# Optimization experiments

Measured on AMD Instinct MI355X. Metric: run time of the kernel, lower is better.

Reference implementation:

```python
import jax, jax.numpy as jnp
import numpy as np

QUANT = 6                      # quant bits
LEVELS = 2 ** QUANT - 1        # quant_levels = 63


def setup_inputs() -> dict:
    key = jax.random.key(0)
    k1, k2, k3 = jax.random.split(key, 3)
    B, C_in, C_out, H, W = 8, 256, 256, 64, 64
    x = jax.random.normal(k1, (B, C_in, H, W), dtype=jnp.float32)
    # 1x1 conv weight stored as [out_channels, in_channels] (kernel dims are 1)
    weight = jax.random.normal(k2, (C_out, C_in), dtype=jnp.float32) * 0.05
    bias = jax.random.normal(k3, (C_out,), dtype=jnp.float32) * 0.05
    return {"x": x, "weight": weight, "bias": bias}


def reference(x, weight, bias):
    """NoiseConv.forward with hard_weight set, mode='batch':
    channel_wise_quantize -> hardware_inference -> float cast.
    (Original computes in float64 on CUDA; here float32 for jit/accel friendliness.)
    """
    # --- channel_wise_quantize (input is detached in torch) ---
    xd = jax.lax.stop_gradient(x)
    cmax = jnp.max(xd, axis=1, keepdims=True)           # [B,1,H,W]
    cmin = jnp.min(xd, axis=1, keepdims=True)           # [B,1,H,W]
    scaling = (cmax - cmin) / LEVELS                    # [B,1,H,W]
    x_int = jnp.round((xd - cmin) / scaling).astype(jnp.int32)  # [B,C,H,W] in [0,63]
    bit_idx = jnp.arange(QUANT, dtype=jnp.int32)
    bits = ((x_int[..., None] >> bit_idx) & 1).astype(x.dtype)   # [B,C,H,W,Q] bitplanes

    # --- hardware_inference (batch mode): one 1x1 conv per bitplane, then
    # weighted recombination with 2^b. Fused here into a single einsum; the
    # math is identical since conv is linear and bitplane values are exact. ---
    base = (2.0 ** jnp.arange(QUANT)).astype(x.dtype)   # quant_base
    out_sum = jnp.einsum('bchwq,q,oc->bohw', bits, base, weight)  # [B,O,H,W]
    out_w = out_sum * scaling                           # per-pixel rescale

    # min-offset term: conv2d(cmin * ones_like(x_plane), weight, bias).
    # cmin is constant across input channels, so it equals cmin * sum_c(w) + bias.
    wsum = jnp.sum(weight, axis=1)                      # [O]
    out_w = out_w + cmin * wsum[None, :, None, None] + bias[None, :, None, None]

    return out_w.astype(jnp.float32)
```

## Files before the change

kernel.cpp:

```cpp
#include <hip/hip_runtime.h>
#include <stdint.h>

#define CI 256
#define CO 256
#define HW 4096
#define PT 64
#define QPAD 72

typedef __attribute__((ext_vector_type(8))) short short8;
typedef __attribute__((ext_vector_type(4))) float float4v;

__global__ void prep_kernel(const float* __restrict__ w,
                            ushort* __restrict__ w16,
                            float* __restrict__ wsum) {
    const int o = blockIdx.x;
    const int lane = threadIdx.x;
    float4 v = ((const float4*)(w + o * CI))[lane];
    auto cvt = [](float f) -> ushort {
        uint32_t u = __float_as_uint(f);
        return (ushort)((u + 0x7FFFu + ((u >> 16) & 1u)) >> 16);
    };
    ushort4 q;
    q.x = cvt(v.x); q.y = cvt(v.y); q.z = cvt(v.z); q.w = cvt(v.w);
    ((ushort4*)(w16 + o * CI))[lane] = q;
    float s = v.x + v.y + v.z + v.w;
    for (int off = 32; off >= 1; off >>= 1) s += __shfl_down(s, off);
    if (lane == 0) wsum[o] = s;
}

__global__ __launch_bounds__(256, 2)
void noise_conv_kernel(const float* __restrict__ x,
                       const ushort* __restrict__ w16,
                       const float* __restrict__ wsum,
                       const float* __restrict__ bias,
                       float* __restrict__ out) {
    __shared__ ushort Qlds[PT][QPAD];
    __shared__ float4 rmin4[16][16];
    __shared__ float4 rmax4[16][16];
    __shared__ float cmin_s[PT], s_s[PT], inv_s[PT];

    const int t = threadIdx.x;
    const int blk = blockIdx.x;
    const int img = blk >> 6;
    const int p0 = (blk & 63) * PT;
    const float* xb = x + (size_t)img * CI * HW + p0;
    float* outb = out + (size_t)img * CO * HW + p0;

    {
        const int pg = t & 15;
        const int slice = t >> 4;
        float4 vmin = make_float4(__builtin_inff(), __builtin_inff(),
                                  __builtin_inff(), __builtin_inff());
        float4 vmax = make_float4(-__builtin_inff(), -__builtin_inff(),
                                  -__builtin_inff(), -__builtin_inff());
        #pragma unroll
        for (int i = 0; i < 16; ++i) {
            const float4 v = ((const float4*)(xb + (size_t)(slice * 16 + i) * HW))[pg];
            vmin.x = fminf(vmin.x, v.x); vmax.x = fmaxf(vmax.x, v.x);
            vmin.y = fminf(vmin.y, v.y); vmax.y = fmaxf(vmax.y, v.y);
            vmin.z = fminf(vmin.z, v.z); vmax.z = fmaxf(vmax.z, v.z);
            vmin.w = fminf(vmin.w, v.w); vmax.w = fmaxf(vmax.w, v.w);
        }
        rmin4[slice][pg] = vmin;
        rmax4[slice][pg] = vmax;
    }
    __syncthreads();
    if (t < 16) {
        float4 mn = rmin4[0][t], mx = rmax4[0][t];
        for (int sl = 1; sl < 16; ++sl) {
            float4 a = rmin4[sl][t], b = rmax4[sl][t];
            mn.x = fminf(mn.x, a.x); mx.x = fmaxf(mx.x, b.x);
            mn.y = fminf(mn.y, a.y); mx.y = fmaxf(mx.y, b.y);
            mn.z = fminf(mn.z, a.z); mx.z = fmaxf(mx.z, b.z);
            mn.w = fminf(mn.w, a.w); mx.w = fmaxf(mx.w, b.w);
        }
        const float mnv[4] = {mn.x, mn.y, mn.z, mn.w};
        const float mxv[4] = {mx.x, mx.y, mx.z, mx.w};
        #pragma unroll
        for (int c = 0; c < 4; ++c) {
            const int p = t * 4 + c;
            const float cmin = mnv[c];
            const float sc = (mxv[c] - cmin) / 63.0f;
            cmin_s[p] = cmin;
            s_s[p] = sc;
            inv_s[p] = 1.0f / sc;
        }
    }
    __syncthreads();

    const int lane = t & 63;
    const int wv = t >> 6;
    const int row16 = lane & 15;
    const int quad = lane >> 4;

    float4v acc[4][4];
    #pragma unroll
    for (int m = 0; m < 4; ++m)
        #pragma unroll
        for (int n = 0; n < 4; ++n) {
            float4v z = {0.0f, 0.0f, 0.0f, 0.0f};
            acc[m][n] = z;
        }

    const int sp = t & 63;
    const int scb = (t >> 6) * 16;
    const float cm = cmin_s[sp];
    const float iv = inv_s[sp];

    for (int c0 = 0; c0 < CI; c0 += 64) {
        #pragma unroll
        for (int jj = 0; jj < 2; ++jj) {
            uint32_t wds[4];
            #pragma unroll
            for (int j2 = 0; j2 < 4; ++j2) {
                const int c = c0 + scb + jj * 8 + j2 * 2;
                const float a0 = xb[(size_t)c * HW + sp];
                const float a1 = xb[(size_t)(c + 1) * HW + sp];
                const float q0 = rintf((a0 - cm) * iv);
                const float q1 = rintf((a1 - cm) * iv);
                const uint32_t b0 = __float_as_uint(q0) >> 16;
                const uint32_t b1 = __float_as_uint(q1) >> 16;
                wds[j2] = b0 | (b1 << 16);
            }
            *((uint4*)&Qlds[sp][scb + jj * 8]) =
                make_uint4(wds[0], wds[1], wds[2], wds[3]);
        }
        __syncthreads();

        #pragma unroll
        for (int ks = 0; ks < 2; ++ks) {
            const int kk = ks * 32 + quad * 8;
            short8 afr[4], bfr[4];
            #pragma unroll
            for (int m = 0; m < 4; ++m) {
                const int o = wv * 64 + m * 16 + row16;
                afr[m] = *((const short8*)(w16 + o * CI + c0 + kk));
            }
            #pragma unroll
            for (int n = 0; n < 4; ++n) {
                bfr[n] = *((const short8*)&Qlds[n * 16 + row16][kk]);
            }
            #pragma unroll
            for (int m = 0; m < 4; ++m)
                #pragma unroll
                for (int n = 0; n < 4; ++n)
                    acc[m][n] = __builtin_amdgcn_mfma_f32_16x16x32_bf16(
                        afr[m], bfr[n], acc[m][n], 0, 0, 0);
        }
        __syncthreads();
    }

    #pragma unroll
    for (int m = 0; m < 4; ++m) {
        const int ob = wv * 64 + m * 16 + quad * 4;
        const float4 w4 = *((const float4*)(wsum + ob));
        const float4 b4 = *((const float4*)(bias + ob));
        const float wr[4] = {w4.x, w4.y, w4.z, w4.w};
        const float br[4] = {b4.x, b4.y, b4.z, b4.w};
        #pragma unroll
        for (int n = 0; n < 4; ++n) {
            const int pl = n * 16 + row16;
            const float sc = s_s[pl];
            const float cm2 = cmin_s[pl];
            float* op = outb + pl;
            #pragma unroll
            for (int r = 0; r < 4; ++r) {
                op[(size_t)(ob + r) * HW] =
                    acc[m][n][r] * sc + cm2 * wr[r] + br[r];
            }
        }
    }
}

extern "C" void kernel_launch(void* const* d_in, const int* in_sizes, int n_in,
                              void* d_out, int out_size, void* d_ws, size_t ws_size,
                              hipStream_t stream) {
    const float* x    = (const float*)d_in[0];
    const float* w    = (const float*)d_in[1];
    const float* bias = (const float*)d_in[2];
    float* out = (float*)d_out;

    ushort* w16 = (ushort*)d_ws;
    float* wsum = (float*)((char*)d_ws + (size_t)CO * CI * sizeof(ushort));

    prep_kernel<<<CO, 64, 0, stream>>>(w, w16, wsum);
    noise_conv_kernel<<<512, 256, 0, stream>>>(x, w16, wsum, bias, out);
}
```

Measured before the change: 99.11 us.

## Keep quantized activations in registers, drop LDS staging and block barriers

Each wave now owns 16 pixels and loads all 256 input channels for them into registers. It computes per-pixel min/max with wave shuffles instead of an LDS reduction and barriers, and feeds quantized bf16 fragments straight into MFMA as the A operand while streaming weights from global/L2. Outputs are written as float4 along pixels after shuffling scale and offset to the matching lanes. This removes LDS traffic and __syncthreads, but uses far more registers (64 floats of x plus 16 accumulators) and reloads the full weight matrix per wave, and the occupancy hint changes.

New measurement: 118.5 us. 19.6% more time.

```diff
diff --git a/kernel.cpp b/kernel.cpp
--- a/kernel.cpp
+++ b/kernel.cpp
@@ -5,7 +5,6 @@
 #define CO 256
 #define HW 4096
 #define PT 64
-#define QPAD 72
 
 typedef __attribute__((ext_vector_type(8))) short short8;
 typedef __attribute__((ext_vector_type(4))) float float4v;
@@ -28,147 +27,92 @@
     if (lane == 0) wsum[o] = s;
 }
 
-__global__ __launch_bounds__(256, 2)
+__global__ __launch_bounds__(256)
 void noise_conv_kernel(const float* __restrict__ x,
                        const ushort* __restrict__ w16,
                        const float* __restrict__ wsum,
                        const float* __restrict__ bias,
                        float* __restrict__ out) {
-    __shared__ ushort Qlds[PT][QPAD];
-    __shared__ float4 rmin4[16][16];
-    __shared__ float4 rmax4[16][16];
-    __shared__ float cmin_s[PT], s_s[PT], inv_s[PT];
+    const int t = threadIdx.x;
+    const int lane = t & 63;
+    const int wv = t >> 6;
+    const int n16 = lane & 15;
+    const int quad = lane >> 4;
 
-    const int t = threadIdx.x;
     const int blk = blockIdx.x;
     const int img = blk >> 6;
     const int p0 = (blk & 63) * PT;
-    const float* xb = x + (size_t)img * CI * HW + p0;
-    float* outb = out + (size_t)img * CO * HW + p0;
+    const int pix = p0 + wv * 16 + n16;
+    const float* xb = x + (size_t)img * CI * HW;
 
-    {
-        const int pg = t & 15;
-        const int slice = t >> 4;
-        float4 vmin = make_float4(__builtin_inff(), __builtin_inff(),
-                                  __builtin_inff(), __builtin_inff());
-        float4 vmax = make_float4(-__builtin_inff(), -__builtin_inff(),
-                                  -__builtin_inff(), -__builtin_inff());
+    float xv[64];
+    #pragma unroll
+    for (int tt = 0; tt < 8; ++tt)
         #pragma unroll
-        for (int i = 0; i < 16; ++i) {
-            const float4 v = ((const float4*)(xb + (size_t)(slice * 16 + i) * HW))[pg];
-            vmin.x = fminf(vmin.x, v.x); vmax.x = fmaxf(vmax.x, v.x);
-            vmin.y = fminf(vmin.y, v.y); vmax.y = fmaxf(vmax.y, v.y);
-            vmin.z = fminf(vmin.z, v.z); vmax.z = fmaxf(vmax.z, v.z);
-            vmin.w = fminf(vmin.w, v.w); vmax.w = fmaxf(vmax.w, v.w);
+        for (int j = 0; j < 8; ++j)
+            xv[tt * 8 + j] = xb[(size_t)(quad * 8 + 32 * tt + j) * HW + pix];
+
+    float mn = xv[0], mx = xv[0];
+    #pragma unroll
+    for (int i = 1; i < 64; ++i) { mn = fminf(mn, xv[i]); mx = fmaxf(mx, xv[i]); }
+    mn = fminf(mn, __shfl_xor(mn, 16));
+    mx = fmaxf(mx, __shfl_xor(mx, 16));
+    mn = fminf(mn, __shfl_xor(mn, 32));
+    mx = fmaxf(mx, __shfl_xor(mx, 32));
+
+    const float cm = mn;
+    const float sc = (mx - mn) / 63.0f;
+    const float iv = 1.0f / sc;
+
+    short8 afr[8];
+    #pragma unroll
+    for (int tt = 0; tt < 8; ++tt) {
+        union { short8 s; uint32_t u[4]; } fr;
+        #pragma unroll
+        for (int j2 = 0; j2 < 4; ++j2) {
+            const float q0 = rintf((xv[tt * 8 + 2 * j2]     - cm) * iv);
+            const float q1 = rintf((xv[tt * 8 + 2 * j2 + 1] - cm) * iv);
+            fr.u[j2] = (__float_as_uint(q0) >> 16) |
+                       (__float_as_uint(q1) & 0xFFFF0000u);
         }
-        rmin4[slice][pg] = vmin;
-        rmax4[slice][pg] = vmax;
+        afr[tt] = fr.s;
     }
-    __syncthreads();
-    if (t < 16) {
-        float4 mn = rmin4[0][t], mx = rmax4[0][t];
-        for (int sl = 1; sl < 16; ++sl) {
-            float4 a = rmin4[sl][t], b = rmax4[sl][t];
-            mn.x = fminf(mn.x, a.x); mx.x = fmaxf(mx.x, b.x);
-            mn.y = fminf(mn.y, a.y); mx.y = fmaxf(mx.y, b.y);
-            mn.z = fminf(mn.z, a.z); mx.z = fmaxf(mx.z, b.z);
-            mn.w = fminf(mn.w, a.w); mx.w = fmaxf(mx.w, b.w);
-        }
-        const float mnv[4] = {mn.x, mn.y, mn.z, mn.w};
-        const float mxv[4] = {mx.x, mx.y, mx.z, mx.w};
+
+    float4v acc[16];
+    #pragma unroll
+    for (int nt = 0; nt < 16; ++nt) {
+        float4v z = {0.0f, 0.0f, 0.0f, 0.0f};
+        acc[nt] = z;
+    }
+    #pragma unroll
+    for (int tt = 0; tt < 8; ++tt) {
+        const short8 af = afr[tt];
         #pragma unroll
-        for (int c = 0; c < 4; ++c) {
-            const int p = t * 4 + c;
-            const float cmin = mnv[c];
-            const float sc = (mxv[c] - cmin) / 63.0f;
-            cmin_s[p] = cmin;
-            s_s[p] = sc;
-            inv_s[p] = 1.0f / sc;
+        for (int nt = 0; nt < 16; ++nt) {
+            const short8 bf = *((const short8*)(
+                w16 + (size_t)(nt * 16 + n16) * CI + tt * 32 + quad * 8));
+            acc[nt] = __builtin_amdgcn_mfma_f32_16x16x32_bf16(af, bf, acc[nt], 0, 0, 0);
         }
     }
-    __syncthreads();
 
-    const int lane = t & 63;
-    const int wv = t >> 6;
-    const int row16 = lane & 15;
-    const int quad = lane >> 4;
-
-    float4v acc[4][4];
+    float sv[4], cv[4];
     #pragma unroll
-    for (int m = 0; m < 4; ++m)
-        #pragma unroll
-        for (int n = 0; n < 4; ++n) {
-            float4v z = {0.0f, 0.0f, 0.0f, 0.0f};
-            acc[m][n] = z;
-        }
-
-    const int sp = t & 63;
-    const int scb = (t >> 6) * 16;
-    const float cm = cmin_s[sp];
-    const float iv = inv_s[sp];
-
-    for (int c0 = 0; c0 < CI; c0 += 64) {
-        #pragma unroll
-        for (int jj = 0; jj < 2; ++jj) {
-            uint32_t wds[4];
-            #pragma unroll
-            for (int j2 = 0; j2 < 4; ++j2) {
-                const int c = c0 + scb + jj * 8 + j2 * 2;
-                const float a0 = xb[(size_t)c * HW + sp];
-                const float a1 = xb[(size_t)(c + 1) * HW + sp];
-                const float q0 = rintf((a0 - cm) * iv);
-                const float q1 = rintf((a1 - cm) * iv);
-                const uint32_t b0 = __float_as_uint(q0) >> 16;
-                const uint32_t b1 = __float_as_uint(q1) >> 16;
-                wds[j2] = b0 | (b1 << 16);
-            }
-            *((uint4*)&Qlds[sp][scb + jj * 8]) =
-                make_uint4(wds[0], wds[1], wds[2], wds[3]);
-        }
-        __syncthreads();
-
-        #pragma unroll
-        for (int ks = 0; ks < 2; ++ks) {
-            const int kk = ks * 32 + quad * 8;
-            short8 afr[4], bfr[4];
-            #pragma unroll
-            for (int m = 0; m < 4; ++m) {
-                const int o = wv * 64 + m * 16 + row16;
-                afr[m] = *((const short8*)(w16 + o * CI + c0 + kk));
-            }
-            #pragma unroll
-            for (int n = 0; n < 4; ++n) {
-                bfr[n] = *((const short8*)&Qlds[n * 16 + row16][kk]);
-            }
-            #pragma unroll
-            for (int m = 0; m < 4; ++m)
-                #pragma unroll
-                for (int n = 0; n < 4; ++n)
-                    acc[m][n] = __builtin_amdgcn_mfma_f32_16x16x32_bf16(
-                        afr[m], bfr[n], acc[m][n], 0, 0, 0);
-        }
-        __syncthreads();
+    for (int r = 0; r < 4; ++r) {
+        sv[r] = __shfl(sc, quad * 4 + r);
+        cv[r] = __shfl(cm, quad * 4 + r);
     }
-
+    float* outb = out + (size_t)img * CO * HW + p0 + wv * 16 + quad * 4;
     #pragma unroll
-    for (int m = 0; m < 4; ++m) {
-        const int ob = wv * 64 + m * 16 + quad * 4;
-        const float4 w4 = *((const float4*)(wsum + ob));
-        const float4 b4 = *((const float4*)(bias + ob));
-        const float wr[4] = {w4.x, w4.y, w4.z, w4.w};
-        const float br[4] = {b4.x, b4.y, b4.z, b4.w};
-        #pragma unroll
-        for (int n = 0; n < 4; ++n) {
-            const int pl = n * 16 + row16;
-            const float sc = s_s[pl];
-            const float cm2 = cmin_s[pl];
-            float* op = outb + pl;
-            #pragma unroll
-            for (int r = 0; r < 4; ++r) {
-                op[(size_t)(ob + r) * HW] =
-                    acc[m][n][r] * sc + cm2 * wr[r] + br[r];
-            }
-        }
+    for (int nt = 0; nt < 16; ++nt) {
+        const int ch = nt * 16 + n16;
+        const float ws = wsum[ch];
+        const float bs = bias[ch];
+        float4 o;
+        o.x = acc[nt][0] * sv[0] + cv[0] * ws + bs;
+        o.y = acc[nt][1] * sv[1] + cv[1] * ws + bs;
+        o.z = acc[nt][2] * sv[2] + cv[2] * ws + bs;
+        o.w = acc[nt][3] * sv[3] + cv[3] * ws + bs;
+        *((float4*)(outb + (size_t)ch * HW)) = o;
     }
 }
 
```
